# Kernel tuning notes

Measured on AMD Instinct MI355X. Metric: run time of the kernel, lower is better.

The kernel has to match this reference:

```python
import jax, jax.numpy as jnp
import numpy as np

T, B, I, H = 2048, 64, 512, 512


def setup_inputs() -> dict:
    key = jax.random.key(0)
    k1, k2, k3, k4, k5 = jax.random.split(key, 5)
    s = 1.0 / np.sqrt(H)  # torch nn.RNN init scale (uniform), use normal*scale for simplicity
    return {
        "x": jax.random.normal(k1, (T, B, I), dtype=jnp.float32),
        "W_ih": jax.random.normal(k2, (H, I), dtype=jnp.float32) * s,
        "W_hh": jax.random.normal(k3, (H, H), dtype=jnp.float32) * s,
        "b_ih": jax.random.normal(k4, (H,), dtype=jnp.float32) * s,
        "b_hh": jax.random.normal(k5, (H,), dtype=jnp.float32) * s,
    }


def reference(x, W_ih, W_hh, b_ih, b_hh):
    # Vanilla tanh RNN, seq-first layout [T, B, I], h0 = zeros.
    # Precompute input projections for all timesteps in one big GEMM.
    xproj = jnp.einsum("tbi,hi->tbh", x, W_ih) + b_ih + b_hh  # [T, B, H]

    def step(h, xp_t):
        h_new = jnp.tanh(xp_t + h @ W_hh.T)  # [B, H]
        return h_new, h_new

    h0 = jnp.zeros((x.shape[1], W_hh.shape[0]), dtype=x.dtype)
    _, out = jax.lax.scan(step, h0, xproj)  # out: [T, B, H]
    return out.reshape(-1, W_hh.shape[0])  # [T*B, H] matching out.view(-1, hidden_size)
```

## Files before the change

### kernel.cpp

```cpp
#include <hip/hip_runtime.h>
#include <hip/hip_bf16.h>

#define T_DIM 2048
#define B_DIM 64
#define I_DIM 512
#define H_DIM 512

typedef float f32x4 __attribute__((ext_vector_type(4)));

union PK { unsigned long long u; float2 f; };

__global__ __launch_bounds__(256) void xproj_gemm(
    const float* __restrict__ A, const float* __restrict__ Bw,
    const float* __restrict__ bih, const float* __restrict__ bhh,
    float* __restrict__ C)
{
    __shared__ float As[16][132];
    __shared__ float Bs[16][132];

    const int bx = blockIdx.x;
    const int bm = bx >> 2;
    const int bn = bx & 3;
    const int tid = threadIdx.x;
    const int tx = tid & 15;
    const int ty = tid >> 4;
    const int mbase = bm * 128;
    const int nbase = bn * 128;

    float acc[8][8] = {};

    for (int kb = 0; kb < 512; kb += 16) {
        #pragma unroll
        for (int s = 0; s < 2; s++) {
            const int slot = tid + s * 256;
            const int row = slot >> 2;
            const int kv  = slot & 3;
            const float4 av = *(const float4*)(A  + (size_t)(mbase + row) * 512 + kb + kv * 4);
            const float4 bv = *(const float4*)(Bw + (size_t)(nbase + row) * 512 + kb + kv * 4);
            As[kv*4+0][row] = av.x; As[kv*4+1][row] = av.y;
            As[kv*4+2][row] = av.z; As[kv*4+3][row] = av.w;
            Bs[kv*4+0][row] = bv.x; Bs[kv*4+1][row] = bv.y;
            Bs[kv*4+2][row] = bv.z; Bs[kv*4+3][row] = bv.w;
        }
        __syncthreads();

        #pragma unroll
        for (int kk = 0; kk < 16; kk++) {
            float a[8], b[8];
            #pragma unroll
            for (int i = 0; i < 8; i++) a[i] = As[kk][ty + 16 * i];
            #pragma unroll
            for (int j = 0; j < 8; j++) b[j] = Bs[kk][tx + 16 * j];
            #pragma unroll
            for (int i = 0; i < 8; i++)
                #pragma unroll
                for (int j = 0; j < 8; j++)
                    acc[i][j] = fmaf(a[i], b[j], acc[i][j]);
        }
        __syncthreads();
    }

    #pragma unroll
    for (int j = 0; j < 8; j++) {
        const int n = nbase + tx + 16 * j;
        const float bias = bih[n] + bhh[n];
        #pragma unroll
        for (int i = 0; i < 8; i++) {
            const int m = mbase + ty + 16 * i;
            C[(size_t)m * 512 + n] = acc[i][j] + bias;
        }
    }
}

__global__ __launch_bounds__(512, 2) void rnn_scan(
    float* __restrict__ out,
    const float* __restrict__ Whh,
    unsigned long long* __restrict__ hxf,
    unsigned long long* __restrict__ hxs)
{
    __shared__ float h_lds[2][576];

    const int bid   = blockIdx.x;
    const int b     = bid & 63;
    const int slice = bid >> 6;
    const int tid = threadIdx.x;
    const int grp = tid >> 4;
    const int g   = tid & 15;
    const int c0  = slice * 128 + grp * 4;

    f32x4 w[32];
    {
        const float* wp = Whh + (size_t)c0 * 512 + g * 32;
        #pragma unroll
        for (int i = 0; i < 4; i++)
            #pragma unroll
            for (int q = 0; q < 8; q++) {
                const float* addr = wp + i * 512 + q * 4;
                asm volatile("global_load_dwordx4 %0, %1, off"
                             : "=v"(w[i * 8 + q]) : "v"(addr));
            }
        asm volatile("s_waitcnt vmcnt(0)");
    }

    const bool writer = (g & 3) == 0;
    const int  wcol   = c0 + ((g >> 2) & 1) + 2 * ((g >> 3) & 1);

    const size_t PAR = (size_t)B_DIM * H_DIM;
    unsigned long long* fw = hxf + (size_t)b * H_DIM + wcol;
    unsigned long long* sw = hxs + (size_t)b * H_DIM + wcol;
    const unsigned long long* fr = hxf + (size_t)b * H_DIM + tid;
    const unsigned long long* sr = hxs + (size_t)b * H_DIM + tid;

    for (int i = tid; i < 1152; i += 512) ((float*)h_lds)[i] = 0.0f;
    __syncthreads();

    float xpc[8];
    if (writer) {
        #pragma unroll
        for (int j = 0; j < 8; j++)
            xpc[j] = out[((size_t)j * B_DIM + b) * H_DIM + wcol];
    }

    for (int tb = 0; tb < T_DIM; tb += 8) {
        float xpn[8];
        #pragma unroll
        for (int j = 0; j < 8; j++) {
            const int t  = tb + j;
            const int p  = j & 1;
            const int np = p ^ 1;
            const float* hbp = h_lds[p] + g * 36;

            float a0 = 0.f, a1 = 0.f, a2 = 0.f, a3 = 0.f;
            #pragma unroll
            for (int q = 0; q < 8; q++) {
                const f32x4 hv = *(const f32x4*)(hbp + q * 4);
                a0 = fmaf(w[q].x,      hv.x, a0); a0 = fmaf(w[q].y,      hv.y, a0);
                a0 = fmaf(w[q].z,      hv.z, a0); a0 = fmaf(w[q].w,      hv.w, a0);
                a1 = fmaf(w[8 + q].x,  hv.x, a1); a1 = fmaf(w[8 + q].y,  hv.y, a1);
                a1 = fmaf(w[8 + q].z,  hv.z, a1); a1 = fmaf(w[8 + q].w,  hv.w, a1);
                a2 = fmaf(w[16 + q].x, hv.x, a2); a2 = fmaf(w[16 + q].y, hv.y, a2);
                a2 = fmaf(w[16 + q].z, hv.z, a2); a2 = fmaf(w[16 + q].w, hv.w, a2);
                a3 = fmaf(w[24 + q].x, hv.x, a3); a3 = fmaf(w[24 + q].y, hv.y, a3);
                a3 = fmaf(w[24 + q].z, hv.z, a3); a3 = fmaf(w[24 + q].w, hv.w, a3);
            }

            float v;
            {
                const bool hi = (g & 8) != 0;
                const float s0 = hi ? a0 : a2;
                const float s1 = hi ? a1 : a3;
                const float r0 = (hi ? a2 : a0) + __shfl_xor(s0, 8, 64);
                const float r1 = (hi ? a3 : a1) + __shfl_xor(s1, 8, 64);
                const bool h4 = (g & 4) != 0;
                const float s2 = h4 ? r0 : r1;
                v = (h4 ? r1 : r0) + __shfl_xor(s2, 4, 64);
                v += __shfl_xor(v, 2, 64);
                v += __shfl_xor(v, 1, 64);
            }

            const float tag = (float)(t + 1);
            float hv_out = 0.f;
            if (writer) {
                const float z = xpc[j] + v;
                const float e = __expf(2.0f * z);
                hv_out = 1.0f - 2.0f / (e + 1.0f);
                PK pk; pk.f.x = hv_out; pk.f.y = tag;
                *(volatile unsigned long long*)(fw + (size_t)np * PAR) = pk.u;
                __hip_atomic_store(sw + (size_t)np * PAR, pk.u,
                                   __ATOMIC_RELAXED, __HIP_MEMORY_SCOPE_AGENT);
            }

            asm volatile("s_waitcnt vmcnt(0)" ::: "memory");

            const unsigned long long* fpoll = fr + (size_t)np * PAR;
            const unsigned long long* spoll = sr + (size_t)np * PAR;
            PK pa, pb;
            asm volatile("global_load_dwordx2 %0, %1, off sc0"
                         : "=v"(pa.u) : "v"(fpoll));
            asm volatile("global_load_dwordx2 %0, %1, off sc0 sc1"
                         : "=v"(pb.u) : "v"(spoll));
            bool have = false;
            float hval = 0.f;
            for (;;) {
                asm volatile("s_waitcnt vmcnt(1)" : "+v"(pa.u) :: "memory");
                if (!have && pa.f.y == tag) { hval = pa.f.x; have = true; }
                if (__all(have)) break;
                asm volatile("global_load_dwordx2 %0, %1, off sc0"
                             : "=v"(pa.u) : "v"(fpoll));
                asm volatile("s_waitcnt vmcnt(1)" : "+v"(pb.u) :: "memory");
                if (!have && pb.f.y == tag) { hval = pb.f.x; have = true; }
                if (__all(have)) break;
                asm volatile("global_load_dwordx2 %0, %1, off sc0 sc1"
                             : "=v"(pb.u) : "v"(spoll));
            }
            asm volatile("s_waitcnt vmcnt(0)" ::: "memory");

            if (writer) {
                out[((size_t)t * B_DIM + b) * H_DIM + wcol] = hv_out;
                if (j == 4) {
                    #pragma unroll
                    for (int q = 0; q < 8; q++) {
                        int rr = tb + 8 + q; if (rr > T_DIM - 1) rr = T_DIM - 1;
                        xpn[q] = out[((size_t)rr * B_DIM + b) * H_DIM + wcol];
                    }
                }
            }

            h_lds[np][(tid >> 5) * 36 + (tid & 31)] = hval;
            __syncthreads();
        }
        if (writer) {
            #pragma unroll
            for (int q = 0; q < 8; q++) xpc[q] = xpn[q];
        }
    }
}

extern "C" void kernel_launch(void* const* d_in, const int* in_sizes, int n_in,
                              void* d_out, int out_size, void* d_ws, size_t ws_size,
                              hipStream_t stream) {
    const float* x    = (const float*)d_in[0];
    const float* W_ih = (const float*)d_in[1];
    const float* W_hh = (const float*)d_in[2];
    const float* b_ih = (const float*)d_in[3];
    const float* b_hh = (const float*)d_in[4];
    float* out = (float*)d_out;

    unsigned long long* hxf = (unsigned long long*)d_ws;
    unsigned long long* hxs = (unsigned long long*)((char*)d_ws + (size_t)2 * B_DIM * H_DIM * 8);

    xproj_gemm<<<dim3(4096), dim3(256), 0, stream>>>(x, W_ih, b_ih, b_hh, out);
    rnn_scan<<<dim3(256), dim3(512), 0, stream>>>(out, W_hh, hxf, hxs);
}
```

Baseline: 4.336 ms.

## Simplify cross-block h exchange: single buffer, local LDS writes, skip own-slice polling

Drops the duplicated fast/slow exchange buffers and publishes each new hidden value through a single agent-scope atomic store. Each block writes its own slice's hidden values straight into LDS, so only threads covering the other three slices spin on global memory, using plain relaxed atomic loads in a per-thread loop instead of the wave-level dual-buffer polling. This removes the blocking vmcnt(0) wait after the stores and the redundant reads of locally produced data, cutting per-step latency on the serial critical path. Without the sc0/sc1 cache-bypass hints, the relaxed loads may have different visibility latency, and waves now diverge inside the spin loop.

New measurement: 3.997 ms. 7.8% less time.

```diff
diff --git a/kernel.cpp b/kernel.cpp
--- a/kernel.cpp
+++ b/kernel.cpp
@@ -75,8 +75,7 @@
 __global__ __launch_bounds__(512, 2) void rnn_scan(
     float* __restrict__ out,
     const float* __restrict__ Whh,
-    unsigned long long* __restrict__ hxf,
-    unsigned long long* __restrict__ hxs)
+    unsigned long long* __restrict__ hx)
 {
     __shared__ float h_lds[2][576];
 
@@ -102,14 +101,21 @@
         asm volatile("s_waitcnt vmcnt(0)");
     }
 
-    const bool writer = (g & 3) == 0;
-    const int  wcol   = c0 + ((g >> 2) & 1) + 2 * ((g >> 3) & 1);
+    const bool writer    = (g & 3) == 0;
+    const int  wcol      = c0 + ((g >> 2) & 1) + 2 * ((g >> 3) & 1);
+    const bool is_reader = (tid >> 7) != slice;
 
     const size_t PAR = (size_t)B_DIM * H_DIM;
-    unsigned long long* fw = hxf + (size_t)b * H_DIM + wcol;
-    unsigned long long* sw = hxs + (size_t)b * H_DIM + wcol;
-    const unsigned long long* fr = hxf + (size_t)b * H_DIM + tid;
-    const unsigned long long* sr = hxs + (size_t)b * H_DIM + tid;
+    unsigned long long* sw0 = hx + (size_t)b * H_DIM + wcol;
+    unsigned long long* sw1 = sw0 + PAR;
+    const unsigned long long* sr0 = hx + (size_t)b * H_DIM + tid;
+    const unsigned long long* sr1 = sr0 + PAR;
+
+    const int lidx = (tid >> 5) * 36 + (tid & 31);
+    const int widx = (wcol >> 5) * 36 + (wcol & 31);
+
+    const float* xbase = out + (size_t)b * H_DIM + wcol;
+    float*       obase = out + (size_t)b * H_DIM + wcol;
 
     for (int i = tid; i < 1152; i += 512) ((float*)h_lds)[i] = 0.0f;
     __syncthreads();
@@ -117,8 +123,8 @@
     float xpc[8];
     if (writer) {
         #pragma unroll
-        for (int j = 0; j < 8; j++)
-            xpc[j] = out[((size_t)j * B_DIM + b) * H_DIM + wcol];
+        for (int q = 0; q < 8; q++)
+            xpc[q] = xbase[(size_t)q * PAR];
     }
 
     for (int tb = 0; tb < T_DIM; tb += 8) {
@@ -126,9 +132,8 @@
         #pragma unroll
         for (int j = 0; j < 8; j++) {
             const int t  = tb + j;
-            const int p  = j & 1;
-            const int np = p ^ 1;
-            const float* hbp = h_lds[p] + g * 36;
+            const int np = (j & 1) ^ 1;
+            const float* hbp = h_lds[j & 1] + g * 36;
 
             float a0 = 0.f, a1 = 0.f, a2 = 0.f, a3 = 0.f;
             #pragma unroll
@@ -159,54 +164,35 @@
             }
 
             const float tag = (float)(t + 1);
-            float hv_out = 0.f;
             if (writer) {
                 const float z = xpc[j] + v;
                 const float e = __expf(2.0f * z);
-                hv_out = 1.0f - 2.0f / (e + 1.0f);
+                const float hv_out = 1.0f - 2.0f / (e + 1.0f);
+                h_lds[np][widx] = hv_out;
                 PK pk; pk.f.x = hv_out; pk.f.y = tag;
-                *(volatile unsigned long long*)(fw + (size_t)np * PAR) = pk.u;
-                __hip_atomic_store(sw + (size_t)np * PAR, pk.u,
+                __hip_atomic_store(np ? sw1 : sw0, pk.u,
                                    __ATOMIC_RELAXED, __HIP_MEMORY_SCOPE_AGENT);
-            }
-
-            asm volatile("s_waitcnt vmcnt(0)" ::: "memory");
-
-            const unsigned long long* fpoll = fr + (size_t)np * PAR;
-            const unsigned long long* spoll = sr + (size_t)np * PAR;
-            PK pa, pb;
-            asm volatile("global_load_dwordx2 %0, %1, off sc0"
-                         : "=v"(pa.u) : "v"(fpoll));
-            asm volatile("global_load_dwordx2 %0, %1, off sc0 sc1"
-                         : "=v"(pb.u) : "v"(spoll));
-            bool have = false;
-            float hval = 0.f;
-            for (;;) {
-                asm volatile("s_waitcnt vmcnt(1)" : "+v"(pa.u) :: "memory");
-                if (!have && pa.f.y == tag) { hval = pa.f.x; have = true; }
-                if (__all(have)) break;
-                asm volatile("global_load_dwordx2 %0, %1, off sc0"
-                             : "=v"(pa.u) : "v"(fpoll));
-                asm volatile("s_waitcnt vmcnt(1)" : "+v"(pb.u) :: "memory");
-                if (!have && pb.f.y == tag) { hval = pb.f.x; have = true; }
-                if (__all(have)) break;
-                asm volatile("global_load_dwordx2 %0, %1, off sc0 sc1"
-                             : "=v"(pb.u) : "v"(spoll));
-            }
-            asm volatile("s_waitcnt vmcnt(0)" ::: "memory");
-
-            if (writer) {
-                out[((size_t)t * B_DIM + b) * H_DIM + wcol] = hv_out;
-                if (j == 4) {
-                    #pragma unroll
-                    for (int q = 0; q < 8; q++) {
-                        int rr = tb + 8 + q; if (rr > T_DIM - 1) rr = T_DIM - 1;
-                        xpn[q] = out[((size_t)rr * B_DIM + b) * H_DIM + wcol];
-                    }
+                obase[(size_t)t * PAR] = hv_out;
+            }
+
+            if (is_reader) {
+                const unsigned long long* poll = np ? sr1 : sr0;
+                PK rk;
+                do {
+                    rk.u = __hip_atomic_load(poll, __ATOMIC_RELAXED,
+                                             __HIP_MEMORY_SCOPE_AGENT);
+                } while (rk.f.y != tag);
+                h_lds[np][lidx] = rk.f.x;
+            }
+
+            if (writer && j == 4) {
+                #pragma unroll
+                for (int q = 0; q < 8; q++) {
+                    int rr = tb + 8 + q; if (rr >= T_DIM) rr = T_DIM - 1;
+                    xpn[q] = xbase[(size_t)rr * PAR];
                 }
             }
 
-            h_lds[np][(tid >> 5) * 36 + (tid & 31)] = hval;
             __syncthreads();
         }
         if (writer) {
@@ -226,9 +212,8 @@
     const float* b_hh = (const float*)d_in[4];
     float* out = (float*)d_out;
 
-    unsigned long long* hxf = (unsigned long long*)d_ws;
-    unsigned long long* hxs = (unsigned long long*)((char*)d_ws + (size_t)2 * B_DIM * H_DIM * 8);
+    unsigned long long* hx = (unsigned long long*)d_ws;
 
     xproj_gemm<<<dim3(4096), dim3(256), 0, stream>>>(x, W_ih, b_ih, b_hh, out);
-    rnn_scan<<<dim3(256), dim3(512), 0, stream>>>(out, W_hh, hxf, hxs);
+    rnn_scan<<<dim3(256), dim3(512), 0, stream>>>(out, W_hh, hx);
 }
```
